# Performance work log

Measured on AMD Instinct MI355X. Metric: run time of the kernel, lower is better.

## Reference

```python
import jax, jax.numpy as jnp
import numpy as np

BQ = 64  # query block size
BK = 64  # key block size
PV_SCALE = 1e-3  # pvthreshd (~0..50) -> prob threshold, mirrors int8 P-quantization cutoff


def setup_inputs() -> dict:
    key = jax.random.key(0)
    ks = jax.random.split(key, 6)
    B, H, L, D = 2, 16, 2048, 64
    q = jax.random.normal(ks[0], (B, H, L, D), jnp.float32)
    k = jax.random.normal(ks[1], (B, H, L, D), jnp.float32)
    v = jax.random.normal(ks[2], (B, H, L, D), jnp.float32)
    # per-head tuned thresholds (init defaults / autotune ranges)
    cdfthreshd = 0.85 + 0.14 * jax.random.uniform(ks[3], (H,), jnp.float32)
    simthreshd1 = jax.random.uniform(ks[4], (H,), jnp.float32, minval=-0.3, maxval=0.5)
    pvthreshd = jax.random.uniform(ks[5], (H,), jnp.float32, minval=15.0, maxval=25.0)
    return dict(q=q, k=k, v=v, cdfthreshd=cdfthreshd,
                simthreshd1=simthreshd1, pvthreshd=pvthreshd)


def _sparse_meansim_attention(q, k, v, cdfthreshd, simthreshd1, pvthreshd):
    B, H, L, D = q.shape
    nqb, nkb = L // BQ, L // BK
    scale = 1.0 / jnp.sqrt(jnp.float32(D))

    # smooth_k: subtract per-(B,H) key mean along sequence
    k = k - k.mean(axis=2, keepdims=True)

    qb = q.reshape(B, H, nqb, BQ, D)
    kb = k.reshape(B, H, nkb, BK, D)
    qm = qb.mean(axis=3)  # [B,H,nqb,D]
    km = kb.mean(axis=3)  # [B,H,nkb,D]

    # mean cosine similarity of queries to their block mean -> pooled (prunable) blocks
    qn = jnp.linalg.norm(qb, axis=-1)            # [B,H,nqb,BQ]
    qmn = jnp.linalg.norm(qm, axis=-1)           # [B,H,nqb]
    cos = jnp.einsum('bhnqd,bhnd->bhnq', qb, qm) / (qn * qmn[..., None] + 1e-6)
    pooled = cos.mean(axis=-1) > simthreshd1[None, :, None]  # [B,H,nqb]

    # block-level score map from pooled means, CDF-based top-mass block selection
    s = jnp.einsum('bhid,bhjd->bhij', qm, km) * scale        # [B,H,nqb,nkb]
    p = jax.nn.softmax(s, axis=-1)
    order = jnp.argsort(-p, axis=-1)
    p_sorted = jnp.take_along_axis(p, order, axis=-1)
    excl_cdf = jnp.cumsum(p_sorted, axis=-1) - p_sorted      # exclusive CDF
    keep_sorted = excl_cdf < cdfthreshd[None, :, None, None]
    keep = jnp.take_along_axis(keep_sorted, jnp.argsort(order, axis=-1), axis=-1)

    sink = (jnp.arange(nkb) == 0)  # attention_sink: always keep first key block
    block_mask = keep | (~pooled)[..., None] | sink          # [B,H,nqb,nkb]

    # full attention restricted to selected blocks
    S = jnp.einsum('bhqd,bhkd->bhqk', q, k) * scale          # [B,H,L,L]
    m = jnp.repeat(jnp.repeat(block_mask, BQ, axis=2), BK, axis=3)
    P = jax.nn.softmax(jnp.where(m, S, -jnp.inf), axis=-1)

    # second-stage PV pruning: skip PV accumulation for negligible prob blocks
    Pb = P.reshape(B, H, nqb, BQ, nkb, BK)
    pv_keep = Pb.max(axis=(3, 5)) >= pvthreshd[None, :, None, None] * PV_SCALE
    pv_keep = pv_keep | sink
    Pb = Pb * pv_keep[:, :, :, None, :, None].astype(P.dtype)

    o = jnp.einsum('bhqk,bhkd->bhqd', Pb.reshape(B, H, L, L), v)
    return o


def reference(q, k, v, cdfthreshd, simthreshd1, pvthreshd):
    return _sparse_meansim_attention(q, k, v, cdfthreshd, simthreshd1, pvthreshd)
```

## Files before the change

### kernel.cpp

```cpp
#include <hip/hip_runtime.h>
#include <hip/hip_bf16.h>
#include <math.h>
#include <stdint.h>

#define B 2
#define H 16
#define L 2048
#define D 64
#define NB 32

typedef unsigned short u16;
typedef unsigned int u32;
typedef __attribute__((ext_vector_type(2))) unsigned int u32x2;
typedef __attribute__((ext_vector_type(4))) unsigned int u32x4;
typedef __attribute__((ext_vector_type(8))) short s16x8;
typedef __attribute__((ext_vector_type(4))) float f32x4;

union FragU { s16x8 v; u32 u[4]; };

__device__ __forceinline__ u32 pkbf(float a, float b) {
  __hip_bfloat162 h = __float22bfloat162_rn(make_float2(a, b));
  union { __hip_bfloat162 h; u32 u; } cv; cv.h = h; return cv.u;
}
__device__ __forceinline__ float bf2f(u32 u16bits) {
  union { u32 u; float f; } c; c.u = u16bits << 16; return c.f;
}
__device__ __forceinline__ void split4(float4 p, u32x2& hi, u32x2& lo) {
  u32 h01 = pkbf(p.x, p.y), h23 = pkbf(p.z, p.w);
  float rx = p.x - bf2f(h01 & 0xffffu);
  float ry = p.y - bf2f(h01 >> 16);
  float rz = p.z - bf2f(h23 & 0xffffu);
  float rw = p.w - bf2f(h23 >> 16);
  hi = (u32x2){h01, h23};
  lo = (u32x2){pkbf(rx, ry), pkbf(rz, rw)};
}
__device__ __forceinline__ int swz(int row, int colb) {
  return (row << 7) + (colb ^ ((row & 7) << 4));
}

__global__ __launch_bounds__(256) void k_prep(const float* __restrict__ k,
                                              const float* __restrict__ v,
                                              float* __restrict__ ksum,
                                              u16* __restrict__ khi_g,
                                              u16* __restrict__ klo_g,
                                              u16* __restrict__ vthi_g,
                                              u16* __restrict__ vtlo_g,
                                              float* __restrict__ kbmax) {
  int blk = blockIdx.x, bh = blk >> 5, j = blk & 31, t = threadIdx.x;
  int lane = t & 63, w = t >> 6;
  __shared__ float vt[64 * 65];
  __shared__ float pk_[4][64];
  __shared__ unsigned bmaxS;
  if (t == 0) bmaxS = 0u;
  size_t base = (size_t)blk * 4096;

  int r0 = t >> 3;
  int c8 = (t & 7) * 8;
  float cs[8] = {0.f, 0.f, 0.f, 0.f, 0.f, 0.f, 0.f, 0.f};
  float rmax = 0.f;
#pragma unroll
  for (int it = 0; it < 2; ++it) {
    int r = r0 + 32 * it;
    const float* kp = k + base + r * 64 + c8;
    float4 f0 = *(const float4*)kp;
    float4 f1 = *(const float4*)(kp + 4);
    u32x2 h0, l0, h1, l1;
    split4(f0, h0, l0); split4(f1, h1, l1);
    *(u32x4*)(khi_g + base + r * 64 + c8) = (u32x4){h0[0], h0[1], h1[0], h1[1]};
    *(u32x4*)(klo_g + base + r * 64 + c8) = (u32x4){l0[0], l0[1], l1[0], l1[1]};
    cs[0] += f0.x; cs[1] += f0.y; cs[2] += f0.z; cs[3] += f0.w;
    cs[4] += f1.x; cs[5] += f1.y; cs[6] += f1.z; cs[7] += f1.w;
    float ssq = f0.x*f0.x + f0.y*f0.y + f0.z*f0.z + f0.w*f0.w
              + f1.x*f1.x + f1.y*f1.y + f1.z*f1.z + f1.w*f1.w;
    ssq += __shfl_xor(ssq, 1); ssq += __shfl_xor(ssq, 2); ssq += __shfl_xor(ssq, 4);
    if ((t & 7) == 0) rmax = fmaxf(rmax, ssq);
    const float* vp = v + base + r * 64 + c8;
    float4 g0 = *(const float4*)vp;
    float4 g1 = *(const float4*)(vp + 4);
    vt[(c8 + 0) * 65 + r] = g0.x;
    vt[(c8 + 1) * 65 + r] = g0.y;
    vt[(c8 + 2) * 65 + r] = g0.z;
    vt[(c8 + 3) * 65 + r] = g0.w;
    vt[(c8 + 4) * 65 + r] = g1.x;
    vt[(c8 + 5) * 65 + r] = g1.y;
    vt[(c8 + 6) * 65 + r] = g1.z;
    vt[(c8 + 7) * 65 + r] = g1.w;
  }
  if ((t & 7) == 0) atomicMax(&bmaxS, __float_as_uint(rmax));
#pragma unroll
  for (int i = 0; i < 8; ++i) {
    cs[i] += __shfl_xor(cs[i], 8);
    cs[i] += __shfl_xor(cs[i], 16);
    cs[i] += __shfl_xor(cs[i], 32);
  }
  if (lane < 8) {
    *(float4*)&pk_[w][lane * 8]     = (float4){cs[0], cs[1], cs[2], cs[3]};
    *(float4*)&pk_[w][lane * 8 + 4] = (float4){cs[4], cs[5], cs[6], cs[7]};
  }
  __syncthreads();
  if (t < 64) ksum[(size_t)blk * 64 + t] = pk_[0][t] + pk_[1][t] + pk_[2][t] + pk_[3][t];
  if (t == 0) kbmax[blk] = __uint_as_float(bmaxS);
#pragma unroll
  for (int it = 0; it < 2; ++it) {
    int idx = t + 256 * it, d = idx >> 3, s8 = (idx & 7) * 8;
    const float* vr = &vt[d * 65 + s8];
    float4 f0 = {vr[0], vr[1], vr[2], vr[3]};
    float4 f1 = {vr[4], vr[5], vr[6], vr[7]};
    u32x2 h0, l0, h1, l1;
    split4(f0, h0, l0); split4(f1, h1, l1);
    size_t o = (size_t)bh * 131072 + (size_t)d * 2048 + j * 64 + s8;
    *(u32x4*)(vthi_g + o) = (u32x4){h0[0], h0[1], h1[0], h1[1]};
    *(u32x4*)(vtlo_g + o) = (u32x4){l0[0], l0[1], l1[0], l1[1]};
  }
}

__global__ __launch_bounds__(256, 3) void k_attn(
    const float* __restrict__ q,
    const float* __restrict__ ksum,
    const u16* __restrict__ khi_g, const u16* __restrict__ klo_g,
    const u16* __restrict__ vthi_g, const u16* __restrict__ vtlo_g,
    const float* __restrict__ cdfthreshd, const float* __restrict__ simthreshd1,
    const float* __restrict__ pvthreshd, const float* __restrict__ kbmax,
    float* __restrict__ out) {
  int blk0 = blockIdx.x;
  int blk = (blk0 & 7) * 128 + (blk0 >> 3);
  int bh = blk >> 5, iq = blk & 31, h = bh & (H - 1);
  int t = threadIdx.x, lane = t & 63, w = t >> 6;
  int m16 = lane & 15, quad = lane >> 4;

  __shared__ __align__(16) uint8_t smem[24608];
  uint8_t* phB = smem;
  uint8_t* plB = smem + 8192;
  uint8_t* qloB = smem + 16384;
  u32*   rbm   = (u32*)smem;
  float* lpart = (float*)(smem + 8448);
  float* qmS   = (float*)(smem + 9472);
  float* MSs   = (float*)(smem + 9728);
  float* linvS = (float*)(smem + 9984);
  int*   flg   = (int*)(smem + 24576);

  const float* qg = q + ((size_t)bh * L + (size_t)iq * 64) * D;
  const u16* kh = khi_g + (size_t)bh * (L * D);
  const u16* kl = klo_g + (size_t)bh * (L * D);
  const u16* vh = vthi_g + (size_t)bh * (L * D);
  const u16* vl = vtlo_g + (size_t)bh * (L * D);

  s16x8 qhf[4][2];
#pragma unroll
  for (int nt = 0; nt < 4; ++nt)
#pragma unroll
    for (int ks = 0; ks < 2; ++ks) {
      const float* p0 = qg + (size_t)(16 * nt + m16) * 64 + ks * 32 + quad * 8;
      float4 a = *(const float4*)p0;
      float4 b2 = *(const float4*)(p0 + 4);
      u32x2 ha, la, hb, lb;
      split4(a, ha, la); split4(b2, hb, lb);
      FragU fh;
      fh.u[0] = ha[0]; fh.u[1] = ha[1]; fh.u[2] = hb[0]; fh.u[3] = hb[1];
      qhf[nt][ks] = fh.v;
      if (w == 0)
        *(u32x4*)(qloB + swz(16 * nt + m16, ks * 64 + quad * 16)) =
            (u32x4){la[0], la[1], lb[0], lb[1]};
    }
  for (int e = t; e < 64 * 33; e += 256) rbm[e] = 0x7F800000u;

  if (w == 0) {
    float s = 0.f;
    for (int r = 0; r < 64; ++r) s += qg[r * 64 + lane];
    qmS[lane] = s * (1.f / 64.f);
  }
  if (w == 1) {
    float m = (lane < 32) ? kbmax[bh * 32 + lane] : 0.f;
    for (int off = 16; off; off >>= 1) m = fmaxf(m, __shfl_xor(m, off, 32));
    if (lane == 0) ((float*)flg)[3] = m;
  }
  __syncthreads();

  bool keepj = false;
  if (w == 0 && lane < 32) {
    int j = lane;
    const float* ksp = ksum + (size_t)bh * NB * 64 + j * 64;
    float sv = 0.f;
    for (int d = 0; d < 64; ++d) sv += qmS[d] * ksp[d];
    sv *= (1.f / 64.f) * 0.125f;
    float mx = sv;
    for (int off = 16; off; off >>= 1) mx = fmaxf(mx, __shfl_xor(mx, off, 32));
    float p = expf(sv - mx);
    float sum = p;
    for (int off = 16; off; off >>= 1) sum += __shfl_xor(sum, off, 32);
    p /= sum;
    float excl = 0.f;
    for (int u = 0; u < 32; ++u) {
      float pu = __shfl(p, u, 32);
      if ((pu > p) || (pu == p && u < j)) excl += pu;
    }
    keepj = excl < cdfthreshd[h];
  }
  if (w == 1) {
    int r = lane;
    float kmax2 = ((float*)flg)[3];
    float dot = 0.f, qn2 = 0.f, qmn2 = 0.f;
    for (int d = 0; d < 64; ++d) {
      float a = qg[r * 64 + d], b2 = qmS[d];
      dot += a * b2; qn2 += a * a; qmn2 += b2 * b2;
    }
    float cs = dot / (sqrtf(qn2) * sqrtf(qmn2) + 1e-6f);
    float su = cs;
    for (int off = 32; off; off >>= 1) su += __shfl_xor(su, off);
    if (lane == 0) flg[0] = (su * (1.f / 64.f)) > simthreshd1[h];
    MSs[r] = sqrtf(qn2 * kmax2) * 0.125f;
  }
  __syncthreads();
  if (w == 0 && lane < 32) {
    bool bit = keepj || !flg[0] || (lane == 0);
    unsigned long long bal = __ballot(bit);
    if (lane == 0) flg[1] = (int)(u32)bal;
  }
  __syncthreads();
  u32 mw = (u32)flg[1];

  float Mq[4];
#pragma unroll
  for (int nt = 0; nt < 4; ++nt) Mq[nt] = MSs[16 * nt + m16];

  float lp[4] = {0.f, 0.f, 0.f, 0.f};
  {
    u32 rm = mw;
    int j = (int)__builtin_ctz(rm); rm &= rm - 1;
    s16x8 ka0[2], ka1[2];
    {
      const u16* kr0 = kh + (size_t)(j * 64 + 16 * w + m16) * 64 + quad * 8;
      const u16* kl0 = kl + (size_t)(j * 64 + 16 * w + m16) * 64 + quad * 8;
#pragma unroll
      for (int ks = 0; ks < 2; ++ks) {
        ka0[ks] = *(const s16x8*)(kr0 + ks * 32);
        ka1[ks] = *(const s16x8*)(kl0 + ks * 32);
      }
    }
    for (;;) {
      f32x4 acc[4];
#pragma unroll
      for (int nt = 0; nt < 4; ++nt) acc[nt] = (f32x4){0.f, 0.f, 0.f, 0.f};
#pragma unroll
      for (int ks = 0; ks < 2; ++ks) {
        s16x8 ql_[4];
#pragma unroll
        for (int nt = 0; nt < 4; ++nt)
          ql_[nt] = *(const s16x8*)(qloB + swz(16 * nt + m16, ks * 64 + quad * 16));
        __builtin_amdgcn_s_setprio(1);
#pragma unroll
        for (int nt = 0; nt < 4; ++nt) {
          acc[nt] = __builtin_amdgcn_mfma_f32_16x16x32_bf16(ka0[ks], qhf[nt][ks], acc[nt], 0, 0, 0);
          acc[nt] = __builtin_amdgcn_mfma_f32_16x16x32_bf16(ka1[ks], qhf[nt][ks], acc[nt], 0, 0, 0);
          acc[nt] = __builtin_amdgcn_mfma_f32_16x16x32_bf16(ka0[ks], ql_[nt], acc[nt], 0, 0, 0);
        }
        __builtin_amdgcn_s_setprio(0);
      }
      int nj = -1;
      s16x8 kn0[2], kn1[2];
      if (rm) {
        nj = (int)__builtin_ctz(rm); rm &= rm - 1;
        const u16* nr = kh + (size_t)(nj * 64 + 16 * w + m16) * 64 + quad * 8;
        const u16* nl = kl + (size_t)(nj * 64 + 16 * w + m16) * 64 + quad * 8;
#pragma unroll
        for (int ks = 0; ks < 2; ++ks) {
          kn0[ks] = *(const s16x8*)(nr + ks * 32);
          kn1[ks] = *(const s16x8*)(nl + ks * 32);
        }
      }
#pragma unroll
      for (int nt = 0; nt < 4; ++nt) {
        float vmax = -1e30f;
#pragma unroll
        for (int reg = 0; reg < 4; ++reg) {
          float s = acc[nt][reg] * 0.125f - Mq[nt];
          lp[nt] += __expf(s);
          vmax = fmaxf(vmax, s);
        }
        vmax = fmaxf(vmax, __shfl_xor(vmax, 16));
        vmax = fmaxf(vmax, __shfl_xor(vmax, 32));
        if (quad == 0)
          atomicMin(rbm + (16 * nt + m16) * 33 + j, __float_as_uint(fmaxf(-vmax, 0.f)));
      }
      if (nj < 0) break;
#pragma unroll
      for (int ks = 0; ks < 2; ++ks) { ka0[ks] = kn0[ks]; ka1[ks] = kn1[ks]; }
      j = nj;
    }
  }
#pragma unroll
  for (int nt = 0; nt < 4; ++nt) {
    float s = lp[nt];
    s += __shfl_xor(s, 16); s += __shfl_xor(s, 32);
    if (quad == 0) lpart[w * 64 + 16 * nt + m16] = s;
  }
  __syncthreads();
  if (t < 64) linvS[t] = 1.f / (lpart[t] + lpart[64 + t] + lpart[128 + t] + lpart[192 + t]);
  __syncthreads();

  if (w == 0 && lane < 32) {
    bool keep = (mw >> lane) & 1u;
    if (keep && lane != 0) {
      float thr = pvthreshd[h] * 1e-3f;
      float mp = 0.f;
      for (int r = 0; r < 64; ++r) {
        float key = __uint_as_float(rbm[r * 33 + lane]);
        mp = fmaxf(mp, __expf(-key) * linvS[r]);
      }
      keep = mp >= thr;
    }
    unsigned long long bal = __ballot(keep);
    if (lane == 0) flg[2] = (int)(u32)bal;
  }
  __syncthreads();
  u32 gm = (u32)flg[2];

  float linq[4];
#pragma unroll
  for (int nt = 0; nt < 4; ++nt) linq[nt] = linvS[16 * nt + m16];

  f32x4 oacc[4];
#pragma unroll
  for (int nt = 0; nt < 4; ++nt) oacc[nt] = (f32x4){0.f, 0.f, 0.f, 0.f};
  {
    u32 rg = gm;
    int j = (int)__builtin_ctz(rg); rg &= rg - 1;
    s16x8 ka0[2], ka1[2];
    {
      const u16* kr0 = kh + (size_t)(j * 64 + 16 * w + m16) * 64 + quad * 8;
      const u16* kl0 = kl + (size_t)(j * 64 + 16 * w + m16) * 64 + quad * 8;
#pragma unroll
      for (int ks = 0; ks < 2; ++ks) {
        ka0[ks] = *(const s16x8*)(kr0 + ks * 32);
        ka1[ks] = *(const s16x8*)(kl0 + ks * 32);
      }
    }
    for (;;) {
      f32x4 acc[4];
#pragma unroll
      for (int nt = 0; nt < 4; ++nt) acc[nt] = (f32x4){0.f, 0.f, 0.f, 0.f};
#pragma unroll
      for (int ks = 0; ks < 2; ++ks) {
        s16x8 ql_[4];
#pragma unroll
        for (int nt = 0; nt < 4; ++nt)
          ql_[nt] = *(const s16x8*)(qloB + swz(16 * nt + m16, ks * 64 + quad * 16));
        __builtin_amdgcn_s_setprio(1);
#pragma unroll
        for (int nt = 0; nt < 4; ++nt) {
          acc[nt] = __builtin_amdgcn_mfma_f32_16x16x32_bf16(ka0[ks], qhf[nt][ks], acc[nt], 0, 0, 0);
          acc[nt] = __builtin_amdgcn_mfma_f32_16x16x32_bf16(ka1[ks], qhf[nt][ks], acc[nt], 0, 0, 0);
          acc[nt] = __builtin_amdgcn_mfma_f32_16x16x32_bf16(ka0[ks], ql_[nt], acc[nt], 0, 0, 0);
        }
        __builtin_amdgcn_s_setprio(0);
      }
      int nj = -1;
      s16x8 kn0[2], kn1[2];
      if (rg) {
        nj = (int)__builtin_ctz(rg); rg &= rg - 1;
        const u16* nr = kh + (size_t)(nj * 64 + 16 * w + m16) * 64 + quad * 8;
        const u16* nl = kl + (size_t)(nj * 64 + 16 * w + m16) * 64 + quad * 8;
#pragma unroll
        for (int ks = 0; ks < 2; ++ks) {
          kn0[ks] = *(const s16x8*)(nr + ks * 32);
          kn1[ks] = *(const s16x8*)(nl + ks * 32);
        }
      }
      __syncthreads();
#pragma unroll
      for (int nt = 0; nt < 4; ++nt) {
        float4 pv;
        pv.x = __expf(acc[nt][0] * 0.125f - Mq[nt]) * linq[nt];
        pv.y = __expf(acc[nt][1] * 0.125f - Mq[nt]) * linq[nt];
        pv.z = __expf(acc[nt][2] * 0.125f - Mq[nt]) * linq[nt];
        pv.w = __expf(acc[nt][3] * 0.125f - Mq[nt]) * linq[nt];
        u32x2 hi, lo; split4(pv, hi, lo);
        int off = swz(16 * nt + m16, 32 * w + 8 * quad);
        *(u32x2*)(phB + off) = hi;
        *(u32x2*)(plB + off) = lo;
      }
      s16x8 va0[2], va1[2];
      {
        const u16* vr0 = vh + (size_t)(16 * w + m16) * L + j * 64 + quad * 8;
        const u16* vl0 = vl + (size_t)(16 * w + m16) * L + j * 64 + quad * 8;
#pragma unroll
        for (int ks = 0; ks < 2; ++ks) {
          va0[ks] = *(const s16x8*)(vr0 + ks * 32);
          va1[ks] = *(const s16x8*)(vl0 + ks * 32);
        }
      }
      __syncthreads();
#pragma unroll
      for (int ks = 0; ks < 2; ++ks)
#pragma unroll
        for (int nt = 0; nt < 4; ++nt) {
          s16x8 pbh = *(const s16x8*)(phB + swz(16 * nt + m16, ks * 64 + quad * 16));
          s16x8 pbl = *(const s16x8*)(plB + swz(16 * nt + m16, ks * 64 + quad * 16));
          __builtin_amdgcn_s_setprio(1);
          oacc[nt] = __builtin_amdgcn_mfma_f32_16x16x32_bf16(va0[ks], pbh, oacc[nt], 0, 0, 0);
          oacc[nt] = __builtin_amdgcn_mfma_f32_16x16x32_bf16(va1[ks], pbh, oacc[nt], 0, 0, 0);
          oacc[nt] = __builtin_amdgcn_mfma_f32_16x16x32_bf16(va0[ks], pbl, oacc[nt], 0, 0, 0);
          __builtin_amdgcn_s_setprio(0);
        }
      if (nj < 0) break;
#pragma unroll
      for (int ks = 0; ks < 2; ++ks) { ka0[ks] = kn0[ks]; ka1[ks] = kn1[ks]; }
      j = nj;
    }
  }

  float* ob = out + ((size_t)bh * L + (size_t)iq * 64) * D;
#pragma unroll
  for (int nt = 0; nt < 4; ++nt)
    *(f32x4*)(ob + (size_t)(16 * nt + m16) * 64 + 16 * w + 4 * quad) = oacc[nt];
}

extern "C" void kernel_launch(void* const* d_in, const int* in_sizes, int n_in,
                              void* d_out, int out_size, void* d_ws, size_t ws_size,
                              hipStream_t stream) {
  (void)in_sizes; (void)n_in; (void)out_size; (void)ws_size;
  const float* q   = (const float*)d_in[0];
  const float* k   = (const float*)d_in[1];
  const float* v   = (const float*)d_in[2];
  const float* cdf = (const float*)d_in[3];
  const float* sim = (const float*)d_in[4];
  const float* pvt = (const float*)d_in[5];
  float* out = (float*)d_out;

  uint8_t* w8 = (uint8_t*)d_ws;
  float* ksum  = (float*)w8;
  float* kbmax = (float*)(w8 + 262144);
  u16* khi_g  = (u16*)(w8 + 266240);
  u16* klo_g  = khi_g + (size_t)B * H * L * D;
  u16* vthi_g = klo_g + (size_t)B * H * L * D;
  u16* vtlo_g = vthi_g + (size_t)B * H * L * D;

  k_prep<<<B * H * NB, 256, 0, stream>>>(k, v, ksum, khi_g, klo_g, vthi_g, vtlo_g, kbmax);
  k_attn<<<B * H * NB, 256, 0, stream>>>(q, ksum, khi_g, klo_g, vthi_g, vtlo_g,
                                         cdf, sim, pvt, kbmax, out);
}
```

Before: 215.5 us.

## Keep P in registers for PV via 16x16x16 MFMA and reduce partial outputs across waves

Each wave now uses its own S-tile key slice directly as the B operand of 16x16x16 bf16 MFMAs against a transposed V fragment. This removes the P round-trip through shared memory and the two barriers per key block. Each wave accumulates a partial 64x64 output over its 16-key slice, and the four waves sum these partials with shared-memory atomics before the 1/l normalization is applied at the final store. Q-hi fragments move from registers to LDS, which lowers register pressure but adds LDS reads. The cost is four times more accumulator registers, narrower V loads, and a final atomic reduction.

```diff
diff --git a/kernel.cpp b/kernel.cpp
--- a/kernel.cpp
+++ b/kernel.cpp
@@ -14,9 +14,26 @@
 typedef __attribute__((ext_vector_type(2))) unsigned int u32x2;
 typedef __attribute__((ext_vector_type(4))) unsigned int u32x4;
 typedef __attribute__((ext_vector_type(8))) short s16x8;
+typedef __attribute__((ext_vector_type(4))) short s16x4;
 typedef __attribute__((ext_vector_type(4))) float f32x4;
 
-union FragU { s16x8 v; u32 u[4]; };
+#define MFMA32(a, b, c) __builtin_amdgcn_mfma_f32_16x16x32_bf16(a, b, c, 0, 0, 0)
+
+#if defined(__has_builtin)
+#if __has_builtin(__builtin_amdgcn_mfma_f32_16x16x16bf16_1k)
+#define HAVE_MFMA16X16 1
+#endif
+#endif
+
+__device__ __forceinline__ f32x4 mfma16(s16x4 a, s16x4 b, f32x4 c) {
+#ifdef HAVE_MFMA16X16
+  return __builtin_amdgcn_mfma_f32_16x16x16bf16_1k(a, b, c, 0, 0, 0);
+#else
+  s16x8 a8 = {a[0], a[1], a[2], a[3], (short)0, (short)0, (short)0, (short)0};
+  s16x8 b8 = {b[0], b[1], b[2], b[3], (short)0, (short)0, (short)0, (short)0};
+  return __builtin_amdgcn_mfma_f32_16x16x32_bf16(a8, b8, c, 0, 0, 0);
+#endif
+}
 
 __device__ __forceinline__ u32 pkbf(float a, float b) {
   __hip_bfloat162 h = __float22bfloat162_rn(make_float2(a, b));
@@ -128,16 +145,16 @@
   int t = threadIdx.x, lane = t & 63, w = t >> 6;
   int m16 = lane & 15, quad = lane >> 4;
 
-  __shared__ __align__(16) uint8_t smem[24608];
-  uint8_t* phB = smem;
-  uint8_t* plB = smem + 8192;
-  uint8_t* qloB = smem + 16384;
-  u32*   rbm   = (u32*)smem;
-  float* lpart = (float*)(smem + 8448);
-  float* qmS   = (float*)(smem + 9472);
-  float* MSs   = (float*)(smem + 9728);
-  float* linvS = (float*)(smem + 9984);
-  int*   flg   = (int*)(smem + 24576);
+  __shared__ __align__(16) uint8_t smem[33312];
+  uint8_t* qhiB = smem;
+  uint8_t* qloB = smem + 8192;
+  u32*   rbm   = (u32*)(smem + 16384);
+  float* lpart = (float*)(smem + 24832);
+  float* qmS   = (float*)(smem + 25856);
+  float* MSs   = (float*)(smem + 26112);
+  float* otile = (float*)(smem + 16384);
+  float* linvS = (float*)(smem + 33024);
+  int*   flg   = (int*)(smem + 33280);
 
   const float* qg = q + ((size_t)bh * L + (size_t)iq * 64) * D;
   const u16* kh = khi_g + (size_t)bh * (L * D);
@@ -145,23 +162,21 @@
   const u16* vh = vthi_g + (size_t)bh * (L * D);
   const u16* vl = vtlo_g + (size_t)bh * (L * D);
 
-  s16x8 qhf[4][2];
-#pragma unroll
-  for (int nt = 0; nt < 4; ++nt)
-#pragma unroll
-    for (int ks = 0; ks < 2; ++ks) {
-      const float* p0 = qg + (size_t)(16 * nt + m16) * 64 + ks * 32 + quad * 8;
-      float4 a = *(const float4*)p0;
-      float4 b2 = *(const float4*)(p0 + 4);
-      u32x2 ha, la, hb, lb;
-      split4(a, ha, la); split4(b2, hb, lb);
-      FragU fh;
-      fh.u[0] = ha[0]; fh.u[1] = ha[1]; fh.u[2] = hb[0]; fh.u[3] = hb[1];
-      qhf[nt][ks] = fh.v;
-      if (w == 0)
-        *(u32x4*)(qloB + swz(16 * nt + m16, ks * 64 + quad * 16)) =
-            (u32x4){la[0], la[1], lb[0], lb[1]};
-    }
+  if (w == 3) {
+#pragma unroll
+    for (int nt = 0; nt < 4; ++nt)
+#pragma unroll
+      for (int ks = 0; ks < 2; ++ks) {
+        const float* p0 = qg + (size_t)(16 * nt + m16) * 64 + ks * 32 + quad * 8;
+        float4 a = *(const float4*)p0;
+        float4 b2 = *(const float4*)(p0 + 4);
+        u32x2 ha, la, hb, lb;
+        split4(a, ha, la); split4(b2, hb, lb);
+        int off = swz(16 * nt + m16, ks * 64 + quad * 16);
+        *(u32x4*)(qhiB + off) = (u32x4){ha[0], ha[1], hb[0], hb[1]};
+        *(u32x4*)(qloB + off) = (u32x4){la[0], la[1], lb[0], lb[1]};
+      }
+  }
   for (int e = t; e < 64 * 33; e += 256) rbm[e] = 0x7F800000u;
 
   if (w == 0) {
@@ -243,16 +258,18 @@
       for (int nt = 0; nt < 4; ++nt) acc[nt] = (f32x4){0.f, 0.f, 0.f, 0.f};
 #pragma unroll
       for (int ks = 0; ks < 2; ++ks) {
-        s16x8 ql_[4];
-#pragma unroll
-        for (int nt = 0; nt < 4; ++nt)
+        s16x8 qh_[4], ql_[4];
+#pragma unroll
+        for (int nt = 0; nt < 4; ++nt) {
+          qh_[nt] = *(const s16x8*)(qhiB + swz(16 * nt + m16, ks * 64 + quad * 16));
           ql_[nt] = *(const s16x8*)(qloB + swz(16 * nt + m16, ks * 64 + quad * 16));
+        }
         __builtin_amdgcn_s_setprio(1);
 #pragma unroll
         for (int nt = 0; nt < 4; ++nt) {
-          acc[nt] = __builtin_amdgcn_mfma_f32_16x16x32_bf16(ka0[ks], qhf[nt][ks], acc[nt], 0, 0, 0);
-          acc[nt] = __builtin_amdgcn_mfma_f32_16x16x32_bf16(ka1[ks], qhf[nt][ks], acc[nt], 0, 0, 0);
-          acc[nt] = __builtin_amdgcn_mfma_f32_16x16x32_bf16(ka0[ks], ql_[nt], acc[nt], 0, 0, 0);
+          acc[nt] = MFMA32(ka0[ks], qh_[nt], acc[nt]);
+          acc[nt] = MFMA32(ka1[ks], qh_[nt], acc[nt]);
+          acc[nt] = MFMA32(ka0[ks], ql_[nt], acc[nt]);
         }
         __builtin_amdgcn_s_setprio(0);
       }
@@ -315,13 +332,14 @@
   __syncthreads();
   u32 gm = (u32)flg[2];
 
-  float linq[4];
-#pragma unroll
-  for (int nt = 0; nt < 4; ++nt) linq[nt] = linvS[16 * nt + m16];
-
-  f32x4 oacc[4];
-#pragma unroll
-  for (int nt = 0; nt < 4; ++nt) oacc[nt] = (f32x4){0.f, 0.f, 0.f, 0.f};
+  for (int e = t; e < 64 * 65; e += 256) otile[e] = 0.f;
+  __syncthreads();
+
+  f32x4 oacc[4][4];
+#pragma unroll
+  for (int nt = 0; nt < 4; ++nt)
+#pragma unroll
+    for (int dt = 0; dt < 4; ++dt) oacc[nt][dt] = (f32x4){0.f, 0.f, 0.f, 0.f};
   {
     u32 rg = gm;
     int j = (int)__builtin_ctz(rg); rg &= rg - 1;
@@ -341,78 +359,94 @@
       for (int nt = 0; nt < 4; ++nt) acc[nt] = (f32x4){0.f, 0.f, 0.f, 0.f};
 #pragma unroll
       for (int ks = 0; ks < 2; ++ks) {
-        s16x8 ql_[4];
-#pragma unroll
-        for (int nt = 0; nt < 4; ++nt)
+        s16x8 qh_[4], ql_[4];
+#pragma unroll
+        for (int nt = 0; nt < 4; ++nt) {
+          qh_[nt] = *(const s16x8*)(qhiB + swz(16 * nt + m16, ks * 64 + quad * 16));
           ql_[nt] = *(const s16x8*)(qloB + swz(16 * nt + m16, ks * 64 + quad * 16));
+        }
         __builtin_amdgcn_s_setprio(1);
 #pragma unroll
         for (int nt = 0; nt < 4; ++nt) {
-          acc[nt] = __builtin_amdgcn_mfma_f32_16x16x32_bf16(ka0[ks], qhf[nt][ks], acc[nt], 0, 0, 0);
-          acc[nt] = __builtin_amdgcn_mfma_f32_16x16x32_bf16(ka1[ks], qhf[nt][ks], acc[nt], 0, 0, 0);
-          acc[nt] = __builtin_amdgcn_mfma_f32_16x16x32_bf16(ka0[ks], ql_[nt], acc[nt], 0, 0, 0);
+          acc[nt] = MFMA32(ka0[ks], qh_[nt], acc[nt]);
+          acc[nt] = MFMA32(ka1[ks], qh_[nt], acc[nt]);
+          acc[nt] = MFMA32(ka0[ks], ql_[nt], acc[nt]);
         }
         __builtin_amdgcn_s_setprio(0);
       }
       int nj = -1;
-      s16x8 kn0[2], kn1[2];
       if (rg) {
         nj = (int)__builtin_ctz(rg); rg &= rg - 1;
         const u16* nr = kh + (size_t)(nj * 64 + 16 * w + m16) * 64 + quad * 8;
         const u16* nl = kl + (size_t)(nj * 64 + 16 * w + m16) * 64 + quad * 8;
 #pragma unroll
         for (int ks = 0; ks < 2; ++ks) {
-          kn0[ks] = *(const s16x8*)(nr + ks * 32);
-          kn1[ks] = *(const s16x8*)(nl + ks * 32);
-        }
-      }
-      __syncthreads();
+          ka0[ks] = *(const s16x8*)(nr + ks * 32);
+          ka1[ks] = *(const s16x8*)(nl + ks * 32);
+        }
+      }
+      s16x4 vhf[4], vlf[4];
+#pragma unroll
+      for (int dt = 0; dt < 4; ++dt) {
+        const u16* vr = vh + (size_t)(16 * dt + m16) * L + j * 64 + 16 * w + quad * 4;
+        const u16* vlr = vl + (size_t)(16 * dt + m16) * L + j * 64 + 16 * w + quad * 4;
+        vhf[dt] = *(const s16x4*)vr;
+        vlf[dt] = *(const s16x4*)vlr;
+      }
+      s16x4 ph[4], pl[4];
 #pragma unroll
       for (int nt = 0; nt < 4; ++nt) {
-        float4 pv;
-        pv.x = __expf(acc[nt][0] * 0.125f - Mq[nt]) * linq[nt];
-        pv.y = __expf(acc[nt][1] * 0.125f - Mq[nt]) * linq[nt];
-        pv.z = __expf(acc[nt][2] * 0.125f - Mq[nt]) * linq[nt];
-        pv.w = __expf(acc[nt][3] * 0.125f - Mq[nt]) * linq[nt];
-        u32x2 hi, lo; split4(pv, hi, lo);
-        int off = swz(16 * nt + m16, 32 * w + 8 * quad);
-        *(u32x2*)(phB + off) = hi;
-        *(u32x2*)(plB + off) = lo;
-      }
-      s16x8 va0[2], va1[2];
-      {
-        const u16* vr0 = vh + (size_t)(16 * w + m16) * L + j * 64 + quad * 8;
-        const u16* vl0 = vl + (size_t)(16 * w + m16) * L + j * 64 + quad * 8;
-#pragma unroll
-        for (int ks = 0; ks < 2; ++ks) {
-          va0[ks] = *(const s16x8*)(vr0 + ks * 32);
-          va1[ks] = *(const s16x8*)(vl0 + ks * 32);
-        }
-      }
-      __syncthreads();
-#pragma unroll
-      for (int ks = 0; ks < 2; ++ks)
+        float e0 = __expf(acc[nt][0] * 0.125f - Mq[nt]);
+        float e1 = __expf(acc[nt][1] * 0.125f - Mq[nt]);
+        float e2 = __expf(acc[nt][2] * 0.125f - Mq[nt]);
+        float e3 = __expf(acc[nt][3] * 0.125f - Mq[nt]);
+        u32 h01 = pkbf(e0, e1), h23 = pkbf(e2, e3);
+        float r0 = e0 - bf2f(h01 & 0xffffu);
+        float r1 = e1 - bf2f(h01 >> 16);
+        float r2 = e2 - bf2f(h23 & 0xffffu);
+        float r3 = e3 - bf2f(h23 >> 16);
+        u32 l01 = pkbf(r0, r1), l23 = pkbf(r2, r3);
+        union { s16x4 v; u32 u[2]; } cp;
+        cp.u[0] = h01; cp.u[1] = h23; ph[nt] = cp.v;
+        cp.u[0] = l01; cp.u[1] = l23; pl[nt] = cp.v;
+      }
+#pragma unroll
+      for (int dt = 0; dt < 4; ++dt) {
+        __builtin_amdgcn_s_setprio(1);
 #pragma unroll
         for (int nt = 0; nt < 4; ++nt) {
-          s16x8 pbh = *(const s16x8*)(phB + swz(16 * nt + m16, ks * 64 + quad * 16));
-          s16x8 pbl = *(const s16x8*)(plB + swz(16 * nt + m16, ks * 64 + quad * 16));
-          __builtin_amdgcn_s_setprio(1);
-          oacc[nt] = __builtin_amdgcn_mfma_f32_16x16x32_bf16(va0[ks], pbh, oacc[nt], 0, 0, 0);
-          oacc[nt] = __builtin_amdgcn_mfma_f32_16x16x32_bf16(va1[ks], pbh, oacc[nt], 0, 0, 0);
-          oacc[nt] = __builtin_amdgcn_mfma_f32_16x16x32_bf16(va0[ks], pbl, oacc[nt], 0, 0, 0);
-          __builtin_amdgcn_s_setprio(0);
-        }
+          oacc[nt][dt] = mfma16(vhf[dt], ph[nt], oacc[nt][dt]);
+          oacc[nt][dt] = mfma16(vlf[dt], ph[nt], oacc[nt][dt]);
+          oacc[nt][dt] = mfma16(vhf[dt], pl[nt], oacc[nt][dt]);
+        }
+        __builtin_amdgcn_s_setprio(0);
+      }
       if (nj < 0) break;
-#pragma unroll
-      for (int ks = 0; ks < 2; ++ks) { ka0[ks] = kn0[ks]; ka1[ks] = kn1[ks]; }
       j = nj;
     }
   }
-
-  float* ob = out + ((size_t)bh * L + (size_t)iq * 64) * D;
 #pragma unroll
   for (int nt = 0; nt < 4; ++nt)
-    *(f32x4*)(ob + (size_t)(16 * nt + m16) * 64 + 16 * w + 4 * quad) = oacc[nt];
+#pragma unroll
+    for (int dt = 0; dt < 4; ++dt)
+#pragma unroll
+      for (int reg = 0; reg < 4; ++reg)
+        atomicAdd(&otile[(16 * nt + m16) * 65 + 16 * dt + quad * 4 + reg],
+                  oacc[nt][dt][reg]);
+  __syncthreads();
+
+  {
+    int r = t >> 2, c0 = (t & 3) * 16;
+    float lin = linvS[r];
+    float* ob = out + ((size_t)bh * L + (size_t)iq * 64 + r) * 64 + c0;
+    const float* src = &otile[r * 65 + c0];
+#pragma unroll
+    for (int g = 0; g < 4; ++g) {
+      float4 vv = {src[4 * g + 0] * lin, src[4 * g + 1] * lin,
+                   src[4 * g + 2] * lin, src[4 * g + 3] * lin};
+      *(float4*)(ob + 4 * g) = vv;
+    }
+  }
 }
 
 extern "C" void kernel_launch(void* const* d_in, const int* in_sizes, int n_in,
```

Measured after the change: 296.2 us. 1.37x slower.
